# Kernel optimization log

Hardware: AMD Instinct MI355X
Metric: run time of the kernel (lower is better)

## Reference

```python
import jax, jax.numpy as jnp
import numpy as np
from jax import lax

B, CIN, H, W = 4096, 3, 64, 64
NVAR = 50

def _lin(x, w, b):
    return jax.nn.relu(x @ w + b)

def setup_inputs() -> dict:
    key = jax.random.key(0)
    ks = jax.random.split(key, 16)
    def rn(k, shape, scale=0.05):
        return jax.random.normal(k, shape, dtype=jnp.float32) * scale
    return {
        "x": jax.random.normal(ks[0], (B, CIN, H, W), dtype=jnp.float32),
        "C": jax.random.uniform(ks[1], (B, NVAR, NVAR), dtype=jnp.float32),
        "conv1_w": rn(ks[2], (32, CIN, 3, 3)), "conv1_b": jnp.zeros((32,), jnp.float32),
        "conv2_w": rn(ks[3], (64, 32, 3, 3)), "conv2_b": jnp.zeros((64,), jnp.float32),
        "enc_w": rn(ks[4], (64, 128)), "enc_b": jnp.zeros((128,), jnp.float32),
        "f1_w": rn(ks[5], (128, NVAR)), "f1_b": jnp.zeros((NVAR,), jnp.float32),
        "f2_w": rn(ks[6], (NVAR, 128)), "f2_b": jnp.zeros((128,), jnp.float32),
        "f3_w": rn(ks[7], (256, 64)), "f3_b": jnp.zeros((64,), jnp.float32),
        "f4_w": rn(ks[8], (64, 64)), "f4_b": jnp.zeros((64,), jnp.float32),
        "f5_w": rn(ks[9], (64, 64)), "f5_b": jnp.zeros((64,), jnp.float32),
        "out_w": rn(ks[10], (64, NVAR)), "out_b": jnp.zeros((NVAR,), jnp.float32),
    }

def reference(x, C, conv1_w, conv1_b, conv2_w, conv2_b, enc_w, enc_b,
              f1_w, f1_b, f2_w, f2_b, f3_w, f3_b, f4_w, f4_b, f5_w, f5_b,
              out_w, out_b):
    dn = ("NCHW", "OIHW", "NCHW")
    # Observation_Encoder_F: conv(s2)->relu->conv(s2)->relu->global mean pool->linear->relu
    h = lax.conv_general_dilated(x, conv1_w, (2, 2), ((1, 1), (1, 1)), dimension_numbers=dn)
    h = jax.nn.relu(h + conv1_b[None, :, None, None])          # [B,32,32,32]
    h = lax.conv_general_dilated(h, conv2_w, (2, 2), ((1, 1), (1, 1)), dimension_numbers=dn)
    h = jax.nn.relu(h + conv2_b[None, :, None, None])          # [B,64,16,16]
    x1 = _lin(h.mean(axis=(2, 3)), enc_w, enc_b)               # [B,128]
    x2 = _lin(x1, f1_w, f1_b)                                  # [B,V]
    # per-sample causal matrix multiply: e[b] = C[b] @ x2[b]
    e = jnp.einsum("bij,bj->bi", C, x2)                        # [B,V]
    x3 = _lin(e, f2_w, f2_b)                                   # [B,128]
    x4 = jnp.concatenate((x1, x3), axis=1)                     # [B,256]
    x5 = _lin(x4, f3_w, f3_b)
    x6 = _lin(x5, f4_w, f4_b)
    x7 = _lin(x6, f5_w, f5_b)
    return jax.nn.softmax(_lin(x7, out_w, out_b), axis=1)      # [B,V]
```

## Files before the change

kernel.cpp:

```cpp
#include <hip/hip_runtime.h>
#include <hip/hip_bf16.h>


typedef __attribute__((ext_vector_type(8)))  short short8;
typedef __attribute__((ext_vector_type(4)))  float floatx4;
typedef __attribute__((ext_vector_type(16))) float floatx16;

#define AS1 __attribute__((address_space(1)))
#define AS3 __attribute__((address_space(3)))

#define BAR_LGKM() asm volatile("s_waitcnt lgkmcnt(0)\ns_barrier" ::: "memory")
#define BAR_FULL() asm volatile("s_waitcnt vmcnt(0) lgkmcnt(0)\ns_barrier" ::: "memory")
#define BAR_VM4()  asm volatile("s_waitcnt vmcnt(4) lgkmcnt(0)\ns_barrier" ::: "memory")
#define BAR_VM5()  asm volatile("s_waitcnt vmcnt(5) lgkmcnt(0)\ns_barrier" ::: "memory")
#define CFENCE()   asm volatile("" ::: "memory")

__device__ __forceinline__ short f2bf(float f) {
    unsigned u = __float_as_uint(f);
    u += 0x7fffu + ((u >> 16) & 1u);
    return (short)(u >> 16);
}

__device__ __forceinline__ unsigned pkbf2(float a, float b) {
    float2 fp; fp.x = a; fp.y = b;
    __hip_bfloat162 bb = __float22bfloat162_rn(fp);
    return *(unsigned*)&bb;
}

#define WS_MLP_B    40960
#define WS_BIAS_B   (40960 + 115712)
#define WS_POOL_B   163840

__global__ void k_prep(const float* __restrict__ cw2, const float* __restrict__ cw1,
                       const float* __restrict__ ew,  const float* __restrict__ w1,
                       const float* __restrict__ w2,  const float* __restrict__ w3,
                       const float* __restrict__ w4,  const float* __restrict__ w5,
                       const float* __restrict__ ow,  const float* __restrict__ eb,
                       const float* __restrict__ b1,  const float* __restrict__ b2,
                       const float* __restrict__ b3,  const float* __restrict__ b4,
                       const float* __restrict__ b5,  const float* __restrict__ ob,
                       short* __restrict__ packw, float* __restrict__ biasout) {
    const int idx = blockIdx.x * 256 + threadIdx.x;
    if (idx < 18432) {
        const int ic  = idx & 31;
        const int oc  = (idx >> 5) & 63;
        const int pos = idx >> 11;
        packw[idx] = f2bf(cw2[oc * 288 + ic * 9 + pos]);
    } else if (idx < 19456) {
        const int j  = idx - 18432;
        const int k  = j & 31;
        const int oc = j >> 5;
        packw[idx] = (k < 27) ? f2bf(cw1[oc * 27 + k]) : (short)0;
    } else if (idx < 77312) {
        const int e = idx - 19456;
        short v;
        if (e < 9216)        { const int n = e / 72,  kk = e - n * 72;
            v = (kk < 64) ? f2bf(ew[kk * 128 + n]) : (short)0; }
        else if (e < 17920)  { const int r = e - 9216;  const int n = r / 136, kk = r - n * 136;
            v = (kk < 128 && n < 50) ? f2bf(w1[kk * 50 + n]) : (short)0; }
        else if (e < 27136)  { const int r = e - 17920; const int n = r / 72,  kk = r - n * 72;
            v = (kk < 50) ? f2bf(w2[kk * 128 + n]) : (short)0; }
        else if (e < 44032)  { const int r = e - 27136; const int n = r / 264, kk = r - n * 264;
            v = (kk < 256) ? f2bf(w3[kk * 64 + n]) : (short)0; }
        else if (e < 48640)  { const int r = e - 44032; const int n = r / 72,  kk = r - n * 72;
            v = (kk < 64) ? f2bf(w4[kk * 64 + n]) : (short)0; }
        else if (e < 53248)  { const int r = e - 48640; const int n = r / 72,  kk = r - n * 72;
            v = (kk < 64) ? f2bf(w5[kk * 64 + n]) : (short)0; }
        else                 { const int r = e - 53248; const int n = r / 72,  kk = r - n * 72;
            v = (kk < 64 && n < 50) ? f2bf(ow[kk * 50 + n]) : (short)0; }
        packw[20480 + e] = v;
    } else if (idx < 77888) {
        const int j = idx - 77312;
        float v;
        if (j < 128)      v = eb[j];
        else if (j < 192) v = (j - 128 < 50) ? b1[j - 128] : 0.f;
        else if (j < 320) v = b2[j - 192];
        else if (j < 384) v = b3[j - 320];
        else if (j < 448) v = b4[j - 384];
        else if (j < 512) v = b5[j - 448];
        else              v = (j - 512 < 50) ? ob[j - 512] : 0.f;
        biasout[j] = v;
    }
}

#define XS_OFF   0
#define XSB_OFF  24576
#define A1_OFF   49920
#define A1STR    80
#define H1_OFF   90880
#define ROWB     2064
#define POOL_OFF 156928
#define SMEM_SZ  157952
#define SPB      16

__global__ __launch_bounds__(512, 1) void k_conv(
    const float* __restrict__ x,    const float* __restrict__ c1b,
    const short* __restrict__ packw, const float* __restrict__ c2b,
    float* __restrict__ pooled)
{
    __shared__ __align__(16) char smem[SMEM_SZ];
    float* xs      = (float*)(smem + XS_OFF);
    float* xsb     = (float*)(smem + XSB_OFF);
    char*  a1      = smem + A1_OFF;
    char*  h1b     = smem + H1_OFF;
    float* poolbuf = (float*)(smem + POOL_OFF);

    const int tid  = threadIdx.x;
    const int lane = tid & 63;
    const int w    = tid >> 6;

    const int col = lane & 31;
    const int ss  = lane >> 5;

    const int nt  = w & 1;
    const int ox2 = lane & 15;
    const int oyb = (lane >> 4) & 1;
    const int ocn = nt * 32 + col;
    const float bias2 = c2b[ocn];

    short8 z8;
    #pragma unroll
    for (int i = 0; i < 8; ++i) z8[i] = 0;

    short8 bfr[9][2];
    #pragma unroll
    for (int pos = 0; pos < 9; ++pos)
        #pragma unroll
        for (int h = 0; h < 2; ++h)
            bfr[pos][h] = *(const short8*)(packw + (pos * 64 + ocn) * 32 + h * 16 + ss * 8);

    const short* w1p = packw + 18432;
    short8 w1f[2];
    #pragma unroll
    for (int k = 0; k < 2; ++k)
        w1f[k] = *(const short8*)(w1p + col * 32 + k * 16 + ss * 8);

    float2 b1p[8];
    #pragma unroll
    for (int rp = 0; rp < 8; ++rp)
        b1p[rp] = *(const float2*)(c1b + ((rp & 1) * 2 + (rp >> 1) * 8 + 4 * ss));

    int  sbv[3][2];
    bool okx[3];
    #pragma unroll
    for (int kx = 0; kx < 3; ++kx) {
        const int ph   = (kx + 1) & 1;
        const int xh   = ox2 - (kx == 0 ? 1 : 0);
        const int slot = ph * 16 + xh;
        const int swz  = (slot >> 1) & 3;
        okx[kx] = (xh >= 0);
        #pragma unroll
        for (int h = 0; h < 2; ++h)
            sbv[kx][h] = slot * 64 + (((ss + 2 * h) ^ swz) << 4);
    }

    const int slotpx = ((col & 1) << 4) + (col >> 1);
    const int wswz   = (slotpx >> 1) & 3;
    const int wbase  = slotpx * 64 + ss * 8;

    auto issueA = [&](int bb) {
        const char* g = (const char*)(x + (size_t)bb * 12288);
        #pragma unroll
        for (int i = 0; i < 3; ++i) {
            const int idx = w * 3 + i;
            const int ic  = idx >> 3, blk = idx & 7;
            const int so  = ic * 16384 + blk * 1024;
            const int dof = ic * 8192  + blk * 1024;
            __builtin_amdgcn_global_load_lds(
                (const AS1 unsigned int*)(g + so + lane * 16),
                (AS3 unsigned int*)(smem + XS_OFF + dof), 16, 0, 0);
        }
    };
    auto issueB = [&](int bb) {
        const char* g = (const char*)(x + (size_t)bb * 12288);
        #pragma unroll
        for (int i = 0; i < 4; ++i) {
            int idx = w * 4 + i;
            if (idx >= 27) idx -= 27;
            const int ic = idx / 9, k = idx - ic * 9;
            const int so  = ic * 16384 + ((k == 0) ? 7936 : 8192 + (k - 1) * 1024);
            const int dof = ic * 8448  + ((k == 0) ? 0    : 256  + (k - 1) * 1024);
            __builtin_amdgcn_global_load_lds(
                (const AS1 unsigned int*)(g + so + lane * 16),
                (AS3 unsigned int*)(smem + XSB_OFF + dof), 16, 0, 0);
        }
    };

    auto im2col = [&](int half) {
        const int p  = tid;
        const int oy = half * 16 + (p >> 5);
        const int ox = p & 31;
        const int bx = 2 * ox;
        float f[32];
        #pragma unroll
        for (int ic = 0; ic < 3; ++ic) {
            #pragma unroll
            for (int ky = 0; ky < 3; ++ky) {
                const int  iy  = 2 * oy + ky - 1;
                const bool oky = iy >= 0;
                const float* rowp = (half == 0)
                    ? xs  + ic * 2048 + (oky ? iy : 0) * 64
                    : xsb + ic * 2112 + (iy - 31) * 64;
                const float2 p12 = *(const float2*)(rowp + bx);
                const float2 pm  = *(const float2*)(rowp + (bx >= 2 ? bx - 2 : 0));
                const int k = ic * 9 + ky * 3;
                f[k + 0] = (oky && ox > 0) ? pm.y : 0.f;
                f[k + 1] = oky ? p12.x : 0.f;
                f[k + 2] = oky ? p12.y : 0.f;
            }
        }
        f[27] = 0.f; f[28] = 0.f; f[29] = 0.f; f[30] = 0.f; f[31] = 0.f;
        unsigned pk[16];
        #pragma unroll
        for (int t = 0; t < 16; ++t) pk[t] = pkbf2(f[2 * t], f[2 * t + 1]);
        uint4* dst = (uint4*)(a1 + p * A1STR);
        dst[0] = make_uint4(pk[0],  pk[1],  pk[2],  pk[3]);
        dst[1] = make_uint4(pk[4],  pk[5],  pk[6],  pk[7]);
        dst[2] = make_uint4(pk[8],  pk[9],  pk[10], pk[11]);
        dst[3] = make_uint4(pk[12], pk[13], pk[14], pk[15]);
    };

    auto conv1_mfma = [&](int half) {
        #pragma unroll
        for (int i = 0; i < 2; ++i) {
            const int t = w * 2 + i;
            const char* abase = a1 + (t * 32 + col) * A1STR + ss * 16;
            const short8 bf0 = *(const short8*)(abase);
            const short8 bf1 = *(const short8*)(abase + 32);
            floatx16 acc;
            #pragma unroll
            for (int r = 0; r < 16; ++r) acc[r] = 0.f;
            acc = __builtin_amdgcn_mfma_f32_32x32x16_bf16(w1f[0], bf0, acc, 0, 0, 0);
            acc = __builtin_amdgcn_mfma_f32_32x32x16_bf16(w1f[1], bf1, acc, 0, 0, 0);
            const int oyg = half * 16 + t;
            char* hb = h1b + oyg * ROWB + wbase;
            #pragma unroll
            for (int rp = 0; rp < 8; ++rp) {
                const unsigned u = pkbf2(fmaxf(acc[2 * rp]     + b1p[rp].x, 0.f),
                                         fmaxf(acc[2 * rp + 1] + b1p[rp].y, 0.f));
                const int off = (((rp >> 1) ^ wswz) << 4) + (rp & 1) * 4;
                *(unsigned*)(hb + off) = u;
            }
        }
    };

    issueA(blockIdx.x);
    issueB(blockIdx.x);
    CFENCE();
    if (lane < 8) pooled[(size_t)blockIdx.x * 64 + w * 8 + lane] = 0.f;
    CFENCE();
    BAR_VM5();
    im2col(0);
    BAR_LGKM();

    #pragma unroll 1
    for (int s = 0; s < SPB; ++s) {
        const int b  = blockIdx.x + (s << 8);
        const int bn = (s + 1 < SPB) ? b + 256 : b;

        issueA(bn);
        conv1_mfma(0);
        BAR_VM4();
        im2col(1);
        conv1_mfma(1);
        BAR_FULL();

        if (s + 1 < SPB) im2col(0);

        const int t0 = w >> 1;
        float pool = 0.f;
        floatx16 acc0, acc1;
        #pragma unroll
        for (int r = 0; r < 16; ++r) { acc0[r] = 0.f; acc1[r] = 0.f; }
        #pragma unroll
        for (int ky = 0; ky < 3; ++ky) {
            #pragma unroll
            for (int kx = 0; kx < 3; ++kx) {
                const int  iy0 = t0 * 4 + oyb * 2 + ky - 1;
                const bool ok0 = okx[kx] && (iy0 >= 0);
                const bool ok1 = okx[kx];
                const int  ba0 = iy0 * ROWB;
                const int  ba1 = ba0 + 16 * ROWB;
                #pragma unroll
                for (int h = 0; h < 2; ++h) {
                    const int so = sbv[kx][h];
                    short8 a0v = ok0 ? *(const short8*)(h1b + ba0 + so) : z8;
                    short8 a1v = ok1 ? *(const short8*)(h1b + ba1 + so) : z8;
                    const short8 bf = bfr[ky * 3 + kx][h];
                    acc0 = __builtin_amdgcn_mfma_f32_32x32x16_bf16(a0v, bf, acc0, 0, 0, 0);
                    acc1 = __builtin_amdgcn_mfma_f32_32x32x16_bf16(a1v, bf, acc1, 0, 0, 0);
                }
            }
        }
        issueB(bn);
        #pragma unroll
        for (int r = 0; r < 16; ++r) {
            pool += fmaxf(acc0[r] + bias2, 0.f);
            pool += fmaxf(acc1[r] + bias2, 0.f);
        }
        pool += __shfl_xor(pool, 32, 64);
        if (lane < 32) poolbuf[w * 32 + lane] = pool;
        BAR_LGKM();
        if (lane < 8) {
            const int ch = w * 8 + lane;
            const int g = ch >> 5, c = ch & 31;
            pooled[(size_t)b * 64 + ch] =
                (poolbuf[(g    ) * 32 + c] + poolbuf[(g + 2) * 32 + c] +
                 poolbuf[(g + 4) * 32 + c] + poolbuf[(g + 6) * 32 + c]) * (1.f / 256.f);
        }
    }
}

#define ML_BIAS_B 115712
#define ML_P_SH   59392
#define ML_A_SH   60544
#define ML_B_SH   64768
#define ML_Z_F    34496
#define ML_SMEM   142336

__global__ __launch_bounds__(256, 1) void k_mlp(
    const char* __restrict__ wsblk,
    const float* __restrict__ pooled, const float* __restrict__ C,
    float* __restrict__ out)
{
    __shared__ __align__(16) char smem[ML_SMEM];
    short*       Sw   = (short*)smem;
    const short* S    = (const short*)smem;
    const float* Bias = (const float*)(smem + ML_BIAS_B);
    float*       Zf   = (float*)smem;

    const int tid    = threadIdx.x;
    const int lane   = tid & 63;
    const int w      = tid >> 6;
    const int n16    = lane & 15;
    const int q      = lane >> 4;
    const int tile16 = blockIdx.x * 16;

    #pragma unroll
    for (int i = 0; i < 29; ++i) {
        const int off = i * 4096 + w * 1024;
        __builtin_amdgcn_global_load_lds(
            (const AS1 unsigned int*)(wsblk + off + lane * 16),
            (AS3 unsigned int*)(smem + off), 16, 0, 0);
    }
    {
        const float4 pv = *(const float4*)(pooled + tile16 * 64 + tid * 4);
        const int s = tid >> 4, k = (tid & 15) * 4;
        uint2 u;
        u.x = pkbf2(pv.x, pv.y);
        u.y = pkbf2(pv.z, pv.w);
        *(uint2*)(Sw + ML_P_SH + s * 72 + k) = u;
    }
    BAR_FULL();

    auto layer = [&](int inOff, int inPitch, int K, int wOff, int nTiles,
                     int biasOff, int outOff, bool isOut) {
        #pragma unroll
        for (int nt = w; nt < nTiles; nt += 4) {
            floatx4 acc;
            acc[0] = 0.f; acc[1] = 0.f; acc[2] = 0.f; acc[3] = 0.f;
            const int kp = K + 8;
            #pragma unroll
            for (int kc = 0; kc < 8; ++kc) {
                if (kc * 32 >= K) break;
                const short8 aF = *(const short8*)(S + inOff + n16 * inPitch + kc * 32 + q * 8);
                const short8 bF = *(const short8*)(S + wOff + (nt * 16 + n16) * kp + kc * 32 + q * 8);
                acc = __builtin_amdgcn_mfma_f32_16x16x32_bf16(aF, bF, acc, 0, 0, 0);
            }
            const int   n  = nt * 16 + n16;
            const float bv = Bias[biasOff + n];
            #pragma unroll
            for (int r = 0; r < 4; ++r) {
                const int   m = q * 4 + r;
                const float v = fmaxf(acc[r] + bv, 0.f);
                if (isOut) Zf[ML_Z_F + m * 68 + n] = (n < 50) ? v : -1e30f;
                else       Sw[outOff + m * 264 + n] = f2bf(v);
            }
        }
    };

    layer(ML_P_SH, 72, 64, 0, 8, 0, ML_A_SH, false);
    BAR_LGKM();
    layer(ML_A_SH, 264, 128, 9216, 4, 128, ML_B_SH, false);
    BAR_LGKM();

    #pragma unroll
    for (int r = 0; r < 4; ++r) {
        const int item = tid + r * 256;
        if (item < 800) {
            const int s = (item * 1311) >> 16;
            const int i = item - s * 50;
            const float* Cp = C + (size_t)(tile16 + s) * 2500 + i * 50;
            float e = 0.f;
            #pragma unroll
            for (int j2 = 0; j2 < 25; ++j2) {
                const float2   cc = *(const float2*)(Cp + 2 * j2);
                const unsigned u  = *(const unsigned*)(S + ML_B_SH + s * 264 + 2 * j2);
                e += cc.x * __uint_as_float(u << 16)
                   + cc.y * __uint_as_float(u & 0xffff0000u);
            }
            Sw[ML_B_SH + s * 264 + 64 + i] = f2bf(e);
        }
    }
    if ((tid & 15) < 14)
        Sw[ML_B_SH + (tid >> 4) * 264 + 64 + 50 + (tid & 15)] = 0;
    BAR_LGKM();

    layer(ML_B_SH + 64, 264, 64, 17920, 8, 192, ML_A_SH + 128, false);
    BAR_LGKM();
    layer(ML_A_SH, 264, 256, 27136, 4, 320, ML_B_SH, false);
    BAR_LGKM();
    layer(ML_B_SH, 264, 64, 44032, 4, 384, ML_B_SH + 64, false);
    BAR_LGKM();
    layer(ML_B_SH + 64, 264, 64, 48640, 4, 448, ML_B_SH + 128, false);
    BAR_LGKM();
    layer(ML_B_SH + 128, 264, 64, 53248, 4, 512, 0, true);
    BAR_LGKM();

    {
        const int s = tid >> 4, g = tid & 15;
        const float4 zv = *(const float4*)(Zf + ML_Z_F + s * 68 + g * 4);
        float m = fmaxf(fmaxf(zv.x, zv.y), fmaxf(zv.z, zv.w));
        #pragma unroll
        for (int o = 8; o > 0; o >>= 1) m = fmaxf(m, __shfl_xor(m, o, 16));
        float4 p;
        p.x = __expf(zv.x - m); p.y = __expf(zv.y - m);
        p.z = __expf(zv.z - m); p.w = __expf(zv.w - m);
        float sum = p.x + p.y + p.z + p.w;
        #pragma unroll
        for (int o = 8; o > 0; o >>= 1) sum += __shfl_xor(sum, o, 16);
        const float inv = 1.f / sum;
        float* po = out + (size_t)(tile16 + s) * 50 + g * 4;
        const int j = g * 4;
        if (j     < 50) po[0] = p.x * inv;
        if (j + 1 < 50) po[1] = p.y * inv;
        if (j + 2 < 50) po[2] = p.z * inv;
        if (j + 3 < 50) po[3] = p.w * inv;
    }
}

extern "C" void kernel_launch(void* const* d_in, const int* in_sizes, int n_in,
                              void* d_out, int out_size, void* d_ws, size_t ws_size,
                              hipStream_t stream) {
    (void)in_sizes; (void)n_in; (void)out_size; (void)ws_size;
    const float* x   = (const float*)d_in[0];
    const float* Cm  = (const float*)d_in[1];
    const float* c1w = (const float*)d_in[2];
    const float* c1b = (const float*)d_in[3];
    const float* c2w = (const float*)d_in[4];
    const float* c2b = (const float*)d_in[5];
    const float* ew  = (const float*)d_in[6];
    const float* ebv = (const float*)d_in[7];
    const float* f1w = (const float*)d_in[8];
    const float* f1b = (const float*)d_in[9];
    const float* f2w = (const float*)d_in[10];
    const float* f2b = (const float*)d_in[11];
    const float* f3w = (const float*)d_in[12];
    const float* f3b = (const float*)d_in[13];
    const float* f4w = (const float*)d_in[14];
    const float* f4b = (const float*)d_in[15];
    const float* f5w = (const float*)d_in[16];
    const float* f5b = (const float*)d_in[17];
    const float* ow  = (const float*)d_in[18];
    const float* ob  = (const float*)d_in[19];

    short* packw   = (short*)d_ws;
    float* biasout = (float*)((char*)d_ws + WS_BIAS_B);
    float* pooled  = (float*)((char*)d_ws + WS_POOL_B);
    const char* wsblk = (const char*)d_ws + WS_MLP_B;
    float* out     = (float*)d_out;

    hipLaunchKernelGGL(k_prep, dim3(305), dim3(256), 0, stream,
                       c2w, c1w, ew, f1w, f2w, f3w, f4w, f5w, ow,
                       ebv, f1b, f2b, f3b, f4b, f5b, ob, packw, biasout);
    hipLaunchKernelGGL(k_conv, dim3(256), dim3(512), 0, stream,
                       x, c1b, packw, c2b, pooled);
    hipLaunchKernelGGL(k_mlp,  dim3(256), dim3(256), 0, stream,
                       wsblk, pooled, Cm, out);
}
```

Before: 356.0 us.

## Reshape conv2 MFMA tiling to share A fragments across both output-channel halves

Conv2 now has each wave cover one row group and both 32-channel halves, so every loaded A fragment from h1 feeds two MFMAs, roughly halving LDS reads for conv2. This keeps both weight sets (bfr0/bfr1) resident in registers, which raises register pressure. The im2col buffer also moves from an 80-byte padded row stride to a k-chunk-planar layout with a smaller footprint, and the conv1 epilogue writes packed uint2 values instead of individual words. The pooling reduction is rewritten to sum across all eight waves per channel.

New measurement: 399.9 us. 1.12x slower.

```diff
diff --git a/kernel.cpp b/kernel.cpp
--- a/kernel.cpp
+++ b/kernel.cpp
@@ -86,11 +86,10 @@
 #define XS_OFF   0
 #define XSB_OFF  24576
 #define A1_OFF   49920
-#define A1STR    80
-#define H1_OFF   90880
+#define H1_OFF   82688
 #define ROWB     2064
-#define POOL_OFF 156928
-#define SMEM_SZ  157952
+#define POOL_OFF 148736
+#define SMEM_SZ  150784
 #define SPB      16
 
 __global__ __launch_bounds__(512, 1) void k_conv(
@@ -112,22 +111,23 @@
     const int col = lane & 31;
     const int ss  = lane >> 5;
 
-    const int nt  = w & 1;
     const int ox2 = lane & 15;
     const int oyb = (lane >> 4) & 1;
-    const int ocn = nt * 32 + col;
-    const float bias2 = c2b[ocn];
+    const float bias2a = c2b[col];
+    const float bias2b = c2b[32 + col];
 
     short8 z8;
     #pragma unroll
     for (int i = 0; i < 8; ++i) z8[i] = 0;
 
-    short8 bfr[9][2];
+    short8 bfr0[9][2], bfr1[9][2];
     #pragma unroll
     for (int pos = 0; pos < 9; ++pos)
         #pragma unroll
-        for (int h = 0; h < 2; ++h)
-            bfr[pos][h] = *(const short8*)(packw + (pos * 64 + ocn) * 32 + h * 16 + ss * 8);
+        for (int h = 0; h < 2; ++h) {
+            bfr0[pos][h] = *(const short8*)(packw + (pos * 64 + col)      * 32 + h * 16 + ss * 8);
+            bfr1[pos][h] = *(const short8*)(packw + (pos * 64 + 32 + col) * 32 + h * 16 + ss * 8);
+        }
 
     const short* w1p = packw + 18432;
     short8 w1f[2];
@@ -213,20 +213,19 @@
         unsigned pk[16];
         #pragma unroll
         for (int t = 0; t < 16; ++t) pk[t] = pkbf2(f[2 * t], f[2 * t + 1]);
-        uint4* dst = (uint4*)(a1 + p * A1STR);
-        dst[0] = make_uint4(pk[0],  pk[1],  pk[2],  pk[3]);
-        dst[1] = make_uint4(pk[4],  pk[5],  pk[6],  pk[7]);
-        dst[2] = make_uint4(pk[8],  pk[9],  pk[10], pk[11]);
-        dst[3] = make_uint4(pk[12], pk[13], pk[14], pk[15]);
+        *(uint4*)(a1 +     0 + p * 16) = make_uint4(pk[0],  pk[1],  pk[2],  pk[3]);
+        *(uint4*)(a1 +  8192 + p * 16) = make_uint4(pk[4],  pk[5],  pk[6],  pk[7]);
+        *(uint4*)(a1 + 16384 + p * 16) = make_uint4(pk[8],  pk[9],  pk[10], pk[11]);
+        *(uint4*)(a1 + 24576 + p * 16) = make_uint4(pk[12], pk[13], pk[14], pk[15]);
     };
 
     auto conv1_mfma = [&](int half) {
         #pragma unroll
         for (int i = 0; i < 2; ++i) {
             const int t = w * 2 + i;
-            const char* abase = a1 + (t * 32 + col) * A1STR + ss * 16;
-            const short8 bf0 = *(const short8*)(abase);
-            const short8 bf1 = *(const short8*)(abase + 32);
+            const int p16 = (t * 32 + col) * 16;
+            const short8 bf0 = *(const short8*)(a1 + ss * 8192 + p16);
+            const short8 bf1 = *(const short8*)(a1 + ss * 8192 + 16384 + p16);
             floatx16 acc;
             #pragma unroll
             for (int r = 0; r < 16; ++r) acc[r] = 0.f;
@@ -235,11 +234,12 @@
             const int oyg = half * 16 + t;
             char* hb = h1b + oyg * ROWB + wbase;
             #pragma unroll
-            for (int rp = 0; rp < 8; ++rp) {
-                const unsigned u = pkbf2(fmaxf(acc[2 * rp]     + b1p[rp].x, 0.f),
-                                         fmaxf(acc[2 * rp + 1] + b1p[rp].y, 0.f));
-                const int off = (((rp >> 1) ^ wswz) << 4) + (rp & 1) * 4;
-                *(unsigned*)(hb + off) = u;
+            for (int j = 0; j < 4; ++j) {
+                const unsigned ua = pkbf2(fmaxf(acc[4 * j]     + b1p[2 * j].x,     0.f),
+                                          fmaxf(acc[4 * j + 1] + b1p[2 * j].y,     0.f));
+                const unsigned ub = pkbf2(fmaxf(acc[4 * j + 2] + b1p[2 * j + 1].x, 0.f),
+                                          fmaxf(acc[4 * j + 3] + b1p[2 * j + 1].y, 0.f));
+                *(uint2*)(hb + ((j ^ wswz) << 4)) = make_uint2(ua, ub);
             }
         }
     };
@@ -267,46 +267,42 @@
 
         if (s + 1 < SPB) im2col(0);
 
-        const int t0 = w >> 1;
-        float pool = 0.f;
-        floatx16 acc0, acc1;
-        #pragma unroll
-        for (int r = 0; r < 16; ++r) { acc0[r] = 0.f; acc1[r] = 0.f; }
+        float poolA = 0.f, poolB = 0.f;
+        floatx16 accA, accB;
+        #pragma unroll
+        for (int r = 0; r < 16; ++r) { accA[r] = 0.f; accB[r] = 0.f; }
         #pragma unroll
         for (int ky = 0; ky < 3; ++ky) {
             #pragma unroll
             for (int kx = 0; kx < 3; ++kx) {
-                const int  iy0 = t0 * 4 + oyb * 2 + ky - 1;
-                const bool ok0 = okx[kx] && (iy0 >= 0);
-                const bool ok1 = okx[kx];
+                const int  iy0 = w * 4 + oyb * 2 + ky - 1;
+                const bool ok  = okx[kx] && (iy0 >= 0);
                 const int  ba0 = iy0 * ROWB;
-                const int  ba1 = ba0 + 16 * ROWB;
                 #pragma unroll
                 for (int h = 0; h < 2; ++h) {
                     const int so = sbv[kx][h];
-                    short8 a0v = ok0 ? *(const short8*)(h1b + ba0 + so) : z8;
-                    short8 a1v = ok1 ? *(const short8*)(h1b + ba1 + so) : z8;
-                    const short8 bf = bfr[ky * 3 + kx][h];
-                    acc0 = __builtin_amdgcn_mfma_f32_32x32x16_bf16(a0v, bf, acc0, 0, 0, 0);
-                    acc1 = __builtin_amdgcn_mfma_f32_32x32x16_bf16(a1v, bf, acc1, 0, 0, 0);
+                    const short8 av = ok ? *(const short8*)(h1b + ba0 + so) : z8;
+                    accA = __builtin_amdgcn_mfma_f32_32x32x16_bf16(av, bfr0[ky * 3 + kx][h], accA, 0, 0, 0);
+                    accB = __builtin_amdgcn_mfma_f32_32x32x16_bf16(av, bfr1[ky * 3 + kx][h], accB, 0, 0, 0);
                 }
             }
         }
         issueB(bn);
         #pragma unroll
         for (int r = 0; r < 16; ++r) {
-            pool += fmaxf(acc0[r] + bias2, 0.f);
-            pool += fmaxf(acc1[r] + bias2, 0.f);
-        }
-        pool += __shfl_xor(pool, 32, 64);
-        if (lane < 32) poolbuf[w * 32 + lane] = pool;
+            poolA += fmaxf(accA[r] + bias2a, 0.f);
+            poolB += fmaxf(accB[r] + bias2b, 0.f);
+        }
+        poolA += __shfl_xor(poolA, 32, 64);
+        poolB += __shfl_xor(poolB, 32, 64);
+        poolbuf[w * 64 + lane] = (lane < 32) ? poolA : poolB;
         BAR_LGKM();
         if (lane < 8) {
             const int ch = w * 8 + lane;
-            const int g = ch >> 5, c = ch & 31;
-            pooled[(size_t)b * 64 + ch] =
-                (poolbuf[(g    ) * 32 + c] + poolbuf[(g + 2) * 32 + c] +
-                 poolbuf[(g + 4) * 32 + c] + poolbuf[(g + 6) * 32 + c]) * (1.f / 256.f);
+            float sum = 0.f;
+            #pragma unroll
+            for (int wv = 0; wv < 8; ++wv) sum += poolbuf[wv * 64 + ch];
+            pooled[(size_t)b * 64 + ch] = sum * (1.f / 256.f);
         }
     }
 }
```
